# Kernel tuning notes

Measured on AMD Instinct MI355X. Metric: run time of the kernel, lower is better.

The kernel has to match this reference:

```python
import jax, jax.numpy as jnp
import numpy as np

DIMS = 1024
HEAD = 16
HEAD_DIM = DIMS // HEAD
MAX_ITERS = 3
THRESH = 0.01   # torch uses self.threshold.item() -> plain float, no grad
FACTOR = 0.1    # torch uses self.factor.item()
EPS = 1e-5


def _ln(x, w):
    # LayerNorm(bias=False): (x-mean)/sqrt(var+eps) * w
    m = jnp.mean(x, axis=-1, keepdims=True)
    xc = x - m
    v = jnp.mean(xc * xc, axis=-1, keepdims=True)
    return xc * jax.lax.rsqrt(v + EPS) * w


def _focus(xw, Wq, bq, Wk, Wv, bv, Wo, bo, lna_w, lnb_w,
           lq_w, lq_b, lk_w, lk_b, lv_w, lv_b):
    # xw: [B, S, DIMS]. NOTE: in the torch code xa is effectively ignored inside
    # create_qkv (k/v are computed from x due to the `xa is not None` branch bug),
    # so each window is pure self-attention on the query window.
    B, S, D = xw.shape
    xn = _ln(xw, lna_w)
    scale = HEAD_DIM ** -0.25
    q = (xn @ Wq.T + bq) * scale
    k = (xn @ Wk.T) * scale          # k Linear has no bias
    v = xn @ Wv.T + bv

    def shp(t):
        return t.reshape(B, S, HEAD, HEAD_DIM).transpose(0, 2, 1, 3)  # [B,h,S,d]

    q, k, v = shp(q), shp(k), shp(v)
    q = _ln(q, lnb_w)
    k = _ln(k, lnb_w)

    causal = jnp.tril(jnp.ones((S, S), dtype=bool))
    neg = jnp.finfo(jnp.float32).min
    inv_sqrt_d = 1.0 / np.sqrt(HEAD_DIM).astype(np.float32)

    q_cur = q
    prev = jnp.zeros_like(q)
    attn_out = jnp.zeros_like(q)
    done = jnp.array(False)

    # eff_span == S here (span_len >= win_size, ctx % win_size == 0), so the
    # [:eff_span] slices in torch are no-ops. Unrolled loop with where-gating
    # reproduces the data-dependent early exit and stays reverse-differentiable.
    for it in range(MAX_ITERS):
        qp = _ln(q_cur @ lq_w.T + lq_b, lnb_w)
        kp = _ln(k @ lk_w.T + lk_b, lnb_w)
        vp = v @ lv_w.T + lv_b
        s = jnp.einsum('bhqd,bhkd->bhqk', qp, kp) * inv_sqrt_d
        s = jnp.where(causal, s, neg)
        a = jax.nn.softmax(s, axis=-1)
        o = jnp.einsum('bhqk,bhkd->bhqd', a, vp)
        # torch: permute(0,2,1,3).flatten(2) -> [B,S,h*d], then (buggy) raw
        # view(B, HEAD, S, HEAD_DIM) with NO transpose; out_proj is NOT applied
        # in this branch. Reproduced faithfully.
        iter_out = (o.transpose(0, 2, 1, 3)
                     .reshape(B, S, HEAD * HEAD_DIM)
                     .reshape(B, HEAD, S, HEAD_DIM))
        diff = jnp.mean(jnp.abs(iter_out - prev))
        conv = jnp.logical_and(diff < THRESH + FACTOR * diff, it > 0)
        attn_out = jnp.where(done, attn_out, iter_out)
        upd = jnp.logical_or(done, conv)
        q_cur = jnp.where(upd, q_cur, q_cur + iter_out)
        prev = jnp.where(upd, prev, iter_out)
        done = upd

    out = attn_out.transpose(0, 2, 1, 3).reshape(B, S, D)
    return out @ Wo.T + bo


def setup_inputs() -> dict:
    key = jax.random.key(0)
    ks = jax.random.split(key, 10)

    def w(k, shape, s=0.02):
        return jax.random.normal(k, shape, dtype=jnp.float32) * s

    return {
        'x': jax.random.normal(ks[0], (4, 4096, DIMS), dtype=jnp.float32),
        'Wq': w(ks[1], (DIMS, DIMS)), 'bq': jnp.zeros((DIMS,), jnp.float32),
        'Wk': w(ks[2], (DIMS, DIMS)),
        'Wv': w(ks[3], (DIMS, DIMS)), 'bv': jnp.zeros((DIMS,), jnp.float32),
        'Wo': w(ks[4], (DIMS, DIMS)), 'bo': jnp.zeros((DIMS,), jnp.float32),
        'lna_w': jnp.ones((DIMS,), jnp.float32),
        'lnb_w': jnp.ones((HEAD_DIM,), jnp.float32),
        'lq_w': w(ks[5], (HEAD_DIM, HEAD_DIM), 0.1), 'lq_b': jnp.zeros((HEAD_DIM,), jnp.float32),
        'lk_w': w(ks[6], (HEAD_DIM, HEAD_DIM), 0.1), 'lk_b': jnp.zeros((HEAD_DIM,), jnp.float32),
        'lv_w': w(ks[7], (HEAD_DIM, HEAD_DIM), 0.1), 'lv_b': jnp.zeros((HEAD_DIM,), jnp.float32),
        'win_size': 512,
        'span_len': 1024,
    }


def reference(x, Wq, bq, Wk, Wv, bv, Wo, bo, lna_w, lnb_w,
              lq_w, lq_b, lk_w, lk_b, lv_w, lv_b, win_size, span_len):
    # span_len only influences eff_span in torch; with span_len >= win_size it
    # has no effect on the math (k/v come from the query window due to the bug).
    b, ctx, dims = x.shape
    nwin = ctx // win_size  # ctx chosen divisible by win_size
    xw = x.reshape(b, nwin, win_size, dims).transpose(1, 0, 2, 3)  # [nwin,B,W,D]
    f = lambda xx: _focus(xx, Wq, bq, Wk, Wv, bv, Wo, bo, lna_w, lnb_w,
                          lq_w, lq_b, lk_w, lk_b, lv_w, lv_b)
    out = jax.vmap(f)(xw)  # per-window convergence test, matching torch
    return out.transpose(1, 0, 2, 3).reshape(b, ctx, dims)
```

## Files before the change

kernel.cpp:

```cpp
#include <hip/hip_runtime.h>
#include <math.h>

#define DIMS   1024
#define NHEAD  16
#define HD     64
#define WIN    512
#define CTX    4096
#define NBATCH 4
#define NROWS  (NBATCH*CTX)
#define NUNITS (NROWS*NHEAD)
#define LNEPS  1e-5f
#define FIXSCALE 16777216.0

typedef __attribute__((ext_vector_type(8))) short bf16x8;
typedef __attribute__((ext_vector_type(4))) float f32x4;

__device__ __forceinline__ float4 ld4(const float* p) { return *reinterpret_cast<const float4*>(p); }
__device__ __forceinline__ void st4(float* p, float4 v) { *reinterpret_cast<float4*>(p) = v; }

__device__ __forceinline__ float wave_sum64(float v) {
#pragma unroll
    for (int off = 32; off; off >>= 1) v += __shfl_xor(v, off, 64);
    return v;
}
__device__ __forceinline__ float grp16_sum(float v) {
    v += __shfl_xor(v, 1, 64);
    v += __shfl_xor(v, 2, 64);
    v += __shfl_xor(v, 4, 64);
    v += __shfl_xor(v, 8, 64);
    return v;
}

__device__ __forceinline__ unsigned bf16_rn_bits(float x) {
    unsigned u = __float_as_uint(x);
    return (u + 0x7fffu + ((u >> 16) & 1u)) >> 16;
}
__device__ __forceinline__ unsigned pack_hl(float x) {
    unsigned h = bf16_rn_bits(x);
    float hf = __uint_as_float(h << 16);
    unsigned l = bf16_rn_bits(x - hf);
    return (h << 16) | (l & 0xffffu);
}

__device__ __forceinline__ unsigned cvtpk_bf16(float a, float b) {
    unsigned r;
    asm volatile("v_cvt_pk_bf16_f32 %0, %1, %2" : "=v"(r) : "v"(a), "v"(b));
    return r;
}
__device__ __forceinline__ void split_pair(float a, float b, unsigned& hw, unsigned& lw) {
    hw = cvtpk_bf16(a, b);
    float ha = __uint_as_float(hw << 16);
    float hb = __uint_as_float(hw & 0xffff0000u);
    lw = cvtpk_bf16(a - ha, b - hb);
}

__device__ __forceinline__ int swzo(int row, int kbyte) {
    return ((row << 7) + kbyte) ^ ((row & 7) << 4);
}

__global__ __launch_bounds__(256)
void ln1024_pack_kernel(const float* __restrict__ x, const float* __restrict__ w,
                        unsigned* __restrict__ outp) {
    int r = blockIdx.x;
    int tid = threadIdx.x;
    const float* xr = x + (size_t)r * DIMS;
    float4 v = ld4(xr + (tid << 2));
    __shared__ float red[8];
    float s = wave_sum64(v.x + v.y + v.z + v.w);
    int wv = tid >> 6, lane = tid & 63;
    if (lane == 0) red[wv] = s;
    __syncthreads();
    float mean = (red[0] + red[1] + red[2] + red[3]) * (1.0f / DIMS);
    float dx = v.x - mean, dy = v.y - mean, dz = v.z - mean, dw = v.w - mean;
    float ss = wave_sum64(dx*dx + dy*dy + dz*dz + dw*dw);
    if (lane == 0) red[4 + wv] = ss;
    __syncthreads();
    float inv = rsqrtf((red[4] + red[5] + red[6] + red[7]) * (1.0f / DIMS) + LNEPS);
    float4 wv4 = ld4(w + (tid << 2));
    uint4 pk;
    pk.x = pack_hl(dx * inv * wv4.x);
    pk.y = pack_hl(dy * inv * wv4.y);
    pk.z = pack_hl(dz * inv * wv4.z);
    pk.w = pack_hl(dw * inv * wv4.w);
    *reinterpret_cast<uint4*>(outp + (size_t)r * DIMS + (tid << 2)) = pk;
}

__global__ __launch_bounds__(256, 2)
void gemm_hl_kernel(const unsigned* __restrict__ Ahl, const float* __restrict__ W,
                    const float* __restrict__ bias, float* __restrict__ Cm,
                    float alpha, int has_bias) {
    __shared__ short Ah[128 * 64], Al[128 * 64], Wh[128 * 64], Wl[128 * 64];
    int tid = threadIdx.x;
    int wid = tid >> 6, lane = tid & 63;
    int wm = (wid >> 1) << 6, wn = (wid & 1) << 6;
    int g4 = lane >> 4, l16 = lane & 15;
    int m0 = blockIdx.x << 7, n0 = blockIdx.y << 7;

    f32x4 acc[4][4] = {};

    int orow[4], okb[4];
#pragma unroll
    for (int j = 0; j < 4; ++j) {
        int oc = tid + (j << 8);
        orow[j] = oc >> 3;
        okb[j] = (oc & 7) << 4;
    }

    for (int k0 = 0; k0 < 1024; k0 += 64) {
        uint4 a0[4], a1[4];
        float4 w0[4], w1[4];
#pragma unroll
        for (int j = 0; j < 4; ++j) {
            const unsigned* ap = Ahl + (size_t)(m0 + orow[j]) * 1024 + k0 + (okb[j] >> 1);
            a0[j] = *reinterpret_cast<const uint4*>(ap);
            a1[j] = *reinterpret_cast<const uint4*>(ap + 4);
            const float* wp = W + (size_t)(n0 + orow[j]) * 1024 + k0 + (okb[j] >> 1);
            w0[j] = *reinterpret_cast<const float4*>(wp);
            w1[j] = *reinterpret_cast<const float4*>(wp + 4);
        }
        __syncthreads();
#pragma unroll
        for (int j = 0; j < 4; ++j) {
            int off = swzo(orow[j], okb[j]);
            uint4 hi, lo;
            hi.x = __byte_perm(a0[j].x, a0[j].y, 0x7632);
            hi.y = __byte_perm(a0[j].z, a0[j].w, 0x7632);
            hi.z = __byte_perm(a1[j].x, a1[j].y, 0x7632);
            hi.w = __byte_perm(a1[j].z, a1[j].w, 0x7632);
            lo.x = __byte_perm(a0[j].x, a0[j].y, 0x5410);
            lo.y = __byte_perm(a0[j].z, a0[j].w, 0x5410);
            lo.z = __byte_perm(a1[j].x, a1[j].y, 0x5410);
            lo.w = __byte_perm(a1[j].z, a1[j].w, 0x5410);
            *reinterpret_cast<uint4*>(reinterpret_cast<char*>(Ah) + off) = hi;
            *reinterpret_cast<uint4*>(reinterpret_cast<char*>(Al) + off) = lo;

            float xs[8];
            *reinterpret_cast<float4*>(&xs[0]) = w0[j];
            *reinterpret_cast<float4*>(&xs[4]) = w1[j];
            uint4 hw4, lw4;
            unsigned* hwp = &hw4.x;
            unsigned* lwp = &lw4.x;
#pragma unroll
            for (int p = 0; p < 4; ++p) {
                unsigned u0 = __float_as_uint(xs[2*p]);
                unsigned u1 = __float_as_uint(xs[2*p + 1]);
                unsigned h0 = (u0 + 0x8000u) >> 16;
                unsigned h1 = (u1 + 0x8000u) >> 16;
                float l0 = xs[2*p]     - __uint_as_float(h0 << 16);
                float l1 = xs[2*p + 1] - __uint_as_float(h1 << 16);
                unsigned lb0 = (__float_as_uint(l0) + 0x8000u) >> 16;
                unsigned lb1 = (__float_as_uint(l1) + 0x8000u) >> 16;
                hwp[p] = h0 | (h1 << 16);
                lwp[p] = lb0 | (lb1 << 16);
            }
            *reinterpret_cast<uint4*>(reinterpret_cast<char*>(Wh) + off) = hw4;
            *reinterpret_cast<uint4*>(reinterpret_cast<char*>(Wl) + off) = lw4;
        }
        __syncthreads();

#pragma unroll
        for (int kk = 0; kk < 2; ++kk) {
            bf16x8 afh[4], afl[4], wfh[4], wfl[4];
#pragma unroll
            for (int mt = 0; mt < 4; ++mt) {
                int row = wm + (mt << 4) + l16;
                int off = ((row << 7) + (kk << 6) + (g4 << 4)) ^ ((row & 7) << 4);
                afh[mt] = *reinterpret_cast<const bf16x8*>(reinterpret_cast<const char*>(Ah) + off);
                afl[mt] = *reinterpret_cast<const bf16x8*>(reinterpret_cast<const char*>(Al) + off);
            }
#pragma unroll
            for (int nt = 0; nt < 4; ++nt) {
                int row = wn + (nt << 4) + l16;
                int off = ((row << 7) + (kk << 6) + (g4 << 4)) ^ ((row & 7) << 4);
                wfh[nt] = *reinterpret_cast<const bf16x8*>(reinterpret_cast<const char*>(Wh) + off);
                wfl[nt] = *reinterpret_cast<const bf16x8*>(reinterpret_cast<const char*>(Wl) + off);
            }
#pragma unroll
            for (int mt = 0; mt < 4; ++mt)
#pragma unroll
                for (int nt = 0; nt < 4; ++nt) {
                    acc[mt][nt] = __builtin_amdgcn_mfma_f32_16x16x32_bf16(afh[mt], wfh[nt], acc[mt][nt], 0, 0, 0);
                    acc[mt][nt] = __builtin_amdgcn_mfma_f32_16x16x32_bf16(afl[mt], wfh[nt], acc[mt][nt], 0, 0, 0);
                    acc[mt][nt] = __builtin_amdgcn_mfma_f32_16x16x32_bf16(afh[mt], wfl[nt], acc[mt][nt], 0, 0, 0);
                }
        }
    }

#pragma unroll
    for (int mt = 0; mt < 4; ++mt)
#pragma unroll
        for (int nt = 0; nt < 4; ++nt) {
            int col = n0 + wn + (nt << 4) + l16;
            float bb = has_bias ? bias[col] : 0.0f;
#pragma unroll
            for (int r = 0; r < 4; ++r) {
                int row = m0 + wm + (mt << 4) + (g4 << 2) + r;
                Cm[(size_t)row * DIMS + col] = alpha * (acc[mt][nt][r] + bb);
            }
        }
}

__global__ __launch_bounds__(256)
void headln_kernel(float* __restrict__ q, float* __restrict__ k,
                   const float* __restrict__ lnw) {
    int gw = (blockIdx.x << 2) + (threadIdx.x >> 6);
    int lane = threadIdx.x & 63;
    size_t idx = ((size_t)gw << 6) + lane;
    float wgt = lnw[lane];
    {
        float v = q[idx];
        float mean = wave_sum64(v) * (1.0f / 64.0f);
        float d = v - mean;
        float var = wave_sum64(d * d) * (1.0f / 64.0f);
        q[idx] = d * rsqrtf(var + LNEPS) * wgt;
    }
    {
        float v = k[idx];
        float mean = wave_sum64(v) * (1.0f / 64.0f);
        float d = v - mean;
        float var = wave_sum64(d * d) * (1.0f / 64.0f);
        k[idx] = d * rsqrtf(var + LNEPS) * wgt;
    }
}

__global__ __launch_bounds__(256)
void proj64_khl_kernel(const float* __restrict__ inp, const float* __restrict__ W,
                       const float* __restrict__ Wb, const float* __restrict__ lnw,
                       unsigned* __restrict__ plane) {
    int u0 = blockIdx.x << 6;
    __shared__ float As[64][68];
    __shared__ float Bs[64][68];
    int tid = threadIdx.x;
    for (int e = tid; e < 4096; e += 256) Bs[e & 63][e >> 6] = W[e];
    for (int e = tid; e < 1024; e += 256) {
        int row = e >> 4;
        int col = (e & 15) << 2;
        float4 v = ld4(inp + ((size_t)(u0 + row) << 6) + col);
        As[col + 0][row] = v.x; As[col + 1][row] = v.y;
        As[col + 2][row] = v.z; As[col + 3][row] = v.w;
    }
    __syncthreads();
    int tm = tid >> 4, tn = tid & 15;
    float acc[4][4] = {};
#pragma unroll
    for (int k = 0; k < 64; ++k) {
        float4 av = ld4(&As[k][tm << 2]);
        float4 bv = ld4(&Bs[k][tn << 2]);
        float aa[4] = {av.x, av.y, av.z, av.w};
        float bb[4] = {bv.x, bv.y, bv.z, bv.w};
#pragma unroll
        for (int mm = 0; mm < 4; ++mm)
#pragma unroll
            for (int nn = 0; nn < 4; ++nn)
                acc[mm][nn] = fmaf(aa[mm], bb[nn], acc[mm][nn]);
    }
    float bb4[4] = {Wb[(tn << 2) + 0], Wb[(tn << 2) + 1], Wb[(tn << 2) + 2], Wb[(tn << 2) + 3]};
    float lw4[4] = {lnw[(tn << 2) + 0], lnw[(tn << 2) + 1], lnw[(tn << 2) + 2], lnw[(tn << 2) + 3]};
#pragma unroll
    for (int mm = 0; mm < 4; ++mm) {
        float o0 = acc[mm][0] + bb4[0], o1 = acc[mm][1] + bb4[1];
        float o2 = acc[mm][2] + bb4[2], o3 = acc[mm][3] + bb4[3];
        float mean = grp16_sum(o0 + o1 + o2 + o3) * (1.0f / 64.0f);
        float d0 = o0 - mean, d1 = o1 - mean, d2 = o2 - mean, d3 = o3 - mean;
        float var = grp16_sum(d0*d0 + d1*d1 + d2*d2 + d3*d3) * (1.0f / 64.0f);
        float inv = rsqrtf(var + LNEPS);
        o0 = d0 * inv * lw4[0]; o1 = d1 * inv * lw4[1];
        o2 = d2 * inv * lw4[2]; o3 = d3 * inv * lw4[3];
        int u_p = u0 + (tm << 2) + mm;
        int r = u_p >> 4, h = u_p & 15;
        int s = r & 511;
        int ua = ((r >> 9) << 4) + h;
        size_t punit = (size_t)ua * 512 + s;
        uint4 pk;
        pk.x = pack_hl(o0); pk.y = pack_hl(o1); pk.z = pack_hl(o2); pk.w = pack_hl(o3);
        *reinterpret_cast<uint4*>(plane + (punit << 6) + (tn << 2)) = pk;
    }
}

__global__ __launch_bounds__(256)
void proj64_vthl_kernel(const float* __restrict__ inp, const float* __restrict__ W,
                        const float* __restrict__ Wb, unsigned* __restrict__ plane) {
    int u0 = blockIdx.x << 6;
    __shared__ float As[64][68];
    __shared__ float Bs[64][68];
    int tid = threadIdx.x;
    for (int e = tid; e < 4096; e += 256) Bs[e & 63][e >> 6] = W[e];
    for (int e = tid; e < 1024; e += 256) {
        int row = e >> 4;
        int col = (e & 15) << 2;
        float4 v = ld4(inp + ((size_t)(u0 + row) << 6) + col);
        As[col + 0][row] = v.x; As[col + 1][row] = v.y;
        As[col + 2][row] = v.z; As[col + 3][row] = v.w;
    }
    __syncthreads();
    int tm = tid >> 4, tn = tid & 15;
    float acc[4][4] = {};
#pragma unroll
    for (int k = 0; k < 64; ++k) {
        float4 av = ld4(&As[k][tm << 2]);
        float4 bv = ld4(&Bs[k][tn << 2]);
        float aa[4] = {av.x, av.y, av.z, av.w};
        float bb[4] = {bv.x, bv.y, bv.z, bv.w};
#pragma unroll
        for (int mm = 0; mm < 4; ++mm)
#pragma unroll
            for (int nn = 0; nn < 4; ++nn)
                acc[mm][nn] = fmaf(aa[mm], bb[nn], acc[mm][nn]);
    }
    float bb4[4] = {Wb[(tn << 2) + 0], Wb[(tn << 2) + 1], Wb[(tn << 2) + 2], Wb[(tn << 2) + 3]};
#pragma unroll
    for (int mm = 0; mm < 4; ++mm) {
        int u_p = u0 + (tm << 2) + mm;
        int r = u_p >> 4, h = u_p & 15;
        int s = r & 511;
        int ua = ((r >> 9) << 4) + h;
        size_t base = ((size_t)(ua * 8 + (s >> 6)) << 12) + (s & 63);
#pragma unroll
        for (int nn = 0; nn < 4; ++nn) {
            int d = (tn << 2) + nn;
            plane[base + ((size_t)d << 6)] = pack_hl(acc[mm][nn] + bb4[nn]);
        }
    }
}

template<int DIFF, int USE_CONV>
__global__ __launch_bounds__(256)
void attn_mfma_kernel(const float* __restrict__ qacc, const unsigned* __restrict__ khl,
                      const unsigned* __restrict__ vthl, float* __restrict__ o_io,
                      const float* __restrict__ lqw, const float* __restrict__ lqb,
                      const float* __restrict__ lnw,
                      unsigned long long* __restrict__ diff_acc,
                      const int* __restrict__ conv) {
    __shared__ short kh[64][72], kl[64][72], vh[64][72], vl[64][72];
    __shared__ float dred[4];

    int blk = blockIdx.x;
    int u = blk & 511;
    int t = 7 - (blk >> 9);
    int h = u & 15;
    int w = (u >> 4) & 7;
    int b = u >> 7;
    if (USE_CONV && conv[w]) return;
    int rowbase = b * CTX + w * WIN;
    int col0 = h * HD;
    int tid = threadIdx.x;
    int wv = tid >> 6;
    int lane = tid & 63;
    int g4 = lane >> 4;
    int qcol = lane & 15;
    int q_loc = (wv << 4) + qcol;
    int selhi = g4 >> 1;

    const unsigned* kbase = khl + (((size_t)u * 512) << 6);
    const unsigned* vbase = vthl + (((size_t)u * 8) << 12);

    uint4 kpre[4], vpre[4];
#pragma unroll
    for (int rr = 0; rr < 4; ++rr) {
        int row = (wv << 4) + (rr << 2) + g4;
        kpre[rr] = *reinterpret_cast<const uint4*>(kbase + ((size_t)row << 6) + (qcol << 2));
        vpre[rr] = *reinterpret_cast<const uint4*>(vbase + ((size_t)row << 6) + (qcol << 2));
    }

#pragma unroll
    for (int rr = 0; rr < 4; ++rr) {
        int row = (wv << 4) + (rr << 2) + g4;
        float4 v = ld4(lqw + (row << 6) + (qcol << 2));
        unsigned h0, l0, h1, l1;
        split_pair(v.x, v.y, h0, l0);
        split_pair(v.z, v.w, h1, l1);
        *reinterpret_cast<uint2*>(&kh[row][qcol << 2]) = make_uint2(h0, h1);
        *reinterpret_cast<uint2*>(&kl[row][qcol << 2]) = make_uint2(l0, l1);
    }

    bf16x8 bqh[2], bql[2];
    {
        const float* qrow = qacc + (size_t)(rowbase + (t << 6) + q_loc) * DIMS + col0;
#pragma unroll
        for (int kb = 0; kb < 2; ++kb) {
            float4 x0 = ld4(qrow + (kb << 5) + (g4 << 3));
            float4 x1 = ld4(qrow + (kb << 5) + (g4 << 3) + 4);
            unsigned hws[4], lws[4];
            split_pair(x0.x, x0.y, hws[0], lws[0]);
            split_pair(x0.z, x0.w, hws[1], lws[1]);
            split_pair(x1.x, x1.y, hws[2], lws[2]);
            split_pair(x1.z, x1.w, hws[3], lws[3]);
#pragma unroll
            for (int p2 = 0; p2 < 4; ++p2) {
                reinterpret_cast<unsigned*>(&bqh[kb])[p2] = hws[p2];
                reinterpret_cast<unsigned*>(&bql[kb])[p2] = lws[p2];
            }
        }
    }
    __syncthreads();

    f32x4 qpa[4] = {{0,0,0,0},{0,0,0,0},{0,0,0,0},{0,0,0,0}};
    __builtin_amdgcn_s_setprio(1);
#pragma unroll
    for (int jt = 0; jt < 4; ++jt) {
        int arow = (jt << 4) + qcol;
#pragma unroll
        for (int kb = 0; kb < 2; ++kb) {
            bf16x8 ah = *reinterpret_cast<const bf16x8*>(&kh[arow][(kb << 5) + (g4 << 3)]);
            bf16x8 al = *reinterpret_cast<const bf16x8*>(&kl[arow][(kb << 5) + (g4 << 3)]);
            qpa[jt] = __builtin_amdgcn_mfma_f32_16x16x32_bf16(ah, bqh[kb], qpa[jt], 0, 0, 0);
            qpa[jt] = __builtin_amdgcn_mfma_f32_16x16x32_bf16(al, bqh[kb], qpa[jt], 0, 0, 0);
            qpa[jt] = __builtin_amdgcn_mfma_f32_16x16x32_bf16(ah, bql[kb], qpa[jt], 0, 0, 0);
        }
    }
    __builtin_amdgcn_s_setprio(0);

    float vals[16];
    float s1 = 0.0f;
#pragma unroll
    for (int jt = 0; jt < 4; ++jt) {
        float4 b4 = ld4(lqb + (jt << 4) + (g4 << 2));
        const float* b4p = reinterpret_cast<const float*>(&b4);
#pragma unroll
        for (int r = 0; r < 4; ++r) {
            float v = qpa[jt][r] + b4p[r];
            vals[(jt << 2) + r] = v;
            s1 += v;
        }
    }
    s1 += __shfl_xor(s1, 16, 64);
    s1 += __shfl_xor(s1, 32, 64);
    float mean = s1 * (1.0f / 64.0f);
    float s2 = 0.0f;
#pragma unroll
    for (int e = 0; e < 16; ++e) { float d = vals[e] - mean; vals[e] = d; s2 += d * d; }
    s2 += __shfl_xor(s2, 16, 64);
    s2 += __shfl_xor(s2, 32, 64);
    float inv = rsqrtf(s2 * (1.0f / 64.0f) + LNEPS);
#pragma unroll
    for (int jt = 0; jt < 4; ++jt) {
        float4 w4 = ld4(lnw + (jt << 4) + (g4 << 2));
        const float* w4p = reinterpret_cast<const float*>(&w4);
#pragma unroll
        for (int r = 0; r < 4; ++r) vals[(jt << 2) + r] *= inv * w4p[r];
    }

    bf16x8 qfh[2], qfl[2];
    {
        unsigned hw[8], lw[8];
#pragma unroll
        for (int jt = 0; jt < 4; ++jt) {
            split_pair(vals[(jt << 2) + 0], vals[(jt << 2) + 1], hw[(jt << 1) + 0], lw[(jt << 1) + 0]);
            split_pair(vals[(jt << 2) + 2], vals[(jt << 2) + 3], hw[(jt << 1) + 1], lw[(jt << 1) + 1]);
        }
#pragma unroll
        for (int kb = 0; kb < 2; ++kb)
#pragma unroll
            for (int ip = 0; ip < 4; ++ip) {
                int srcl = (((g4 & 1) << 1) + (ip >> 1)) * 16 + qcol;
                unsigned hA = __shfl(hw[(kb << 2) + (ip & 1)], srcl, 64);
                unsigned hB = __shfl(hw[(kb << 2) + 2 + (ip & 1)], srcl, 64);
                unsigned lA = __shfl(lw[(kb << 2) + (ip & 1)], srcl, 64);
                unsigned lB = __shfl(lw[(kb << 2) + 2 + (ip & 1)], srcl, 64);
                reinterpret_cast<unsigned*>(&qfh[kb])[ip] = selhi ? hB : hA;
                reinterpret_cast<unsigned*>(&qfl[kb])[ip] = selhi ? lB : lA;
            }
    }
    __syncthreads();

    float m_r = -INFINITY, l_r = 0.0f;
    f32x4 oacc[4] = {{0,0,0,0},{0,0,0,0},{0,0,0,0},{0,0,0,0}};

    for (int c = 0; c <= t; ++c) {
#pragma unroll
        for (int rr = 0; rr < 4; ++rr) {
            int row = (wv << 4) + (rr << 2) + g4;
            uint4 pk = kpre[rr];
            unsigned* khp = reinterpret_cast<unsigned*>(&kh[row][qcol << 2]);
            khp[0] = __byte_perm(pk.x, pk.y, 0x7632);
            khp[1] = __byte_perm(pk.z, pk.w, 0x7632);
            unsigned* klp = reinterpret_cast<unsigned*>(&kl[row][qcol << 2]);
            klp[0] = __byte_perm(pk.x, pk.y, 0x5410);
            klp[1] = __byte_perm(pk.z, pk.w, 0x5410);
            uint4 pv = vpre[rr];
            unsigned* vhp = reinterpret_cast<unsigned*>(&vh[row][qcol << 2]);
            vhp[0] = __byte_perm(pv.x, pv.y, 0x7632);
            vhp[1] = __byte_perm(pv.z, pv.w, 0x7632);
            unsigned* vlp = reinterpret_cast<unsigned*>(&vl[row][qcol << 2]);
            vlp[0] = __byte_perm(pv.x, pv.y, 0x5410);
            vlp[1] = __byte_perm(pv.z, pv.w, 0x5410);
        }
        if (c < t) {
            const unsigned* ksrc = kbase + (((size_t)(c + 1) * 64) << 6);
            const unsigned* vsrc = vbase + (((size_t)(c + 1)) << 12);
#pragma unroll
            for (int rr = 0; rr < 4; ++rr) {
                int row = (wv << 4) + (rr << 2) + g4;
                kpre[rr] = *reinterpret_cast<const uint4*>(ksrc + ((size_t)row << 6) + (qcol << 2));
                vpre[rr] = *reinterpret_cast<const uint4*>(vsrc + ((size_t)row << 6) + (qcol << 2));
            }
        }
        __syncthreads();

        f32x4 sacc[4] = {{0,0,0,0},{0,0,0,0},{0,0,0,0},{0,0,0,0}};
        __builtin_amdgcn_s_setprio(1);
#pragma unroll
        for (int jt = 0; jt < 4; ++jt) {
            int jrow = (jt << 4) + qcol;
#pragma unroll
            for (int kb = 0; kb < 2; ++kb) {
                bf16x8 ah = *reinterpret_cast<const bf16x8*>(&kh[jrow][(kb << 5) + (g4 << 3)]);
                bf16x8 al = *reinterpret_cast<const bf16x8*>(&kl[jrow][(kb << 5) + (g4 << 3)]);
                sacc[jt] = __builtin_amdgcn_mfma_f32_16x16x32_bf16(ah, qfh[kb], sacc[jt], 0, 0, 0);
                sacc[jt] = __builtin_amdgcn_mfma_f32_16x16x32_bf16(al, qfh[kb], sacc[jt], 0, 0, 0);
                sacc[jt] = __builtin_amdgcn_mfma_f32_16x16x32_bf16(ah, qfl[kb], sacc[jt], 0, 0, 0);
            }
        }
        __builtin_amdgcn_s_setprio(0);

        float sv[16];
        float mx = -3.0e38f;
#pragma unroll
        for (int jt = 0; jt < 4; ++jt)
#pragma unroll
            for (int r = 0; r < 4; ++r) {
                float s = sacc[jt][r] * 0.125f;
                if (c == t) {
                    int j_loc = (jt << 4) + (g4 << 2) + r;
                    if (j_loc > q_loc) s = -3.0e38f;
                }
                sv[(jt << 2) + r] = s;
                mx = fmaxf(mx, s);
            }
        mx = fmaxf(mx, __shfl_xor(mx, 16, 64));
        mx = fmaxf(mx, __shfl_xor(mx, 32, 64));
        float mnew = fmaxf(m_r, mx);
        float ps = 0.0f;
#pragma unroll
        for (int e = 0; e < 16; ++e) {
            float p = __expf(sv[e] - mnew);
            sv[e] = p;
            ps += p;
        }
        ps += __shfl_xor(ps, 16, 64);
        ps += __shfl_xor(ps, 32, 64);
        float ef = __expf(m_r - mnew);
        l_r = l_r * ef + ps;
        m_r = mnew;
#pragma unroll
        for (int dt = 0; dt < 4; ++dt) oacc[dt] *= ef;

        unsigned hwp[8], lwp[8];
#pragma unroll
        for (int jt = 0; jt < 4; ++jt) {
            split_pair(sv[(jt << 2) + 0], sv[(jt << 2) + 1], hwp[(jt << 1) + 0], lwp[(jt << 1) + 0]);
            split_pair(sv[(jt << 2) + 2], sv[(jt << 2) + 3], hwp[(jt << 1) + 1], lwp[(jt << 1) + 1]);
        }

        __builtin_amdgcn_s_setprio(1);
#pragma unroll
        for (int kb2 = 0; kb2 < 2; ++kb2) {
            bf16x8 ph, pl;
#pragma unroll
            for (int ip = 0; ip < 4; ++ip) {
                int srcl = (((g4 & 1) << 1) + (ip >> 1)) * 16 + qcol;
                unsigned hA = __shfl(hwp[(kb2 << 2) + (ip & 1)], srcl, 64);
                unsigned hB = __shfl(hwp[(kb2 << 2) + 2 + (ip & 1)], srcl, 64);
                unsigned lA = __shfl(lwp[(kb2 << 2) + (ip & 1)], srcl, 64);
                unsigned lB = __shfl(lwp[(kb2 << 2) + 2 + (ip & 1)], srcl, 64);
                reinterpret_cast<unsigned*>(&ph)[ip] = selhi ? hB : hA;
                reinterpret_cast<unsigned*>(&pl)[ip] = selhi ? lB : lA;
            }
#pragma unroll
            for (int dt = 0; dt < 4; ++dt) {
                int drow = (dt << 4) + qcol;
                bf16x8 ah = *reinterpret_cast<const bf16x8*>(&vh[drow][(kb2 << 5) + (g4 << 3)]);
                bf16x8 al = *reinterpret_cast<const bf16x8*>(&vl[drow][(kb2 << 5) + (g4 << 3)]);
                oacc[dt] = __builtin_amdgcn_mfma_f32_16x16x32_bf16(ah, ph, oacc[dt], 0, 0, 0);
                oacc[dt] = __builtin_amdgcn_mfma_f32_16x16x32_bf16(al, ph, oacc[dt], 0, 0, 0);
                oacc[dt] = __builtin_amdgcn_mfma_f32_16x16x32_bf16(ah, pl, oacc[dt], 0, 0, 0);
            }
        }
        __builtin_amdgcn_s_setprio(0);
        __syncthreads();
    }

    float invl = 1.0f / l_r;
    float dsum = 0.0f;
    float* orow = o_io + (size_t)(rowbase + (t << 6) + q_loc) * DIMS + col0;
#pragma unroll
    for (int dt = 0; dt < 4; ++dt) {
        float4 ov = make_float4(oacc[dt][0] * invl, oacc[dt][1] * invl,
                                oacc[dt][2] * invl, oacc[dt][3] * invl);
        float* addr = orow + (dt << 4) + (g4 << 2);
        if (DIFF) {
            float4 pv4 = ld4(addr);
            dsum += fabsf(ov.x - pv4.x) + fabsf(ov.y - pv4.y)
                  + fabsf(ov.z - pv4.z) + fabsf(ov.w - pv4.w);
        }
        st4(addr, ov);
    }
    if (DIFF) {
        float s = wave_sum64(dsum);
        if (lane == 0) dred[wv] = s;
        __syncthreads();
        if (tid == 0) {
            double tot = (double)(dred[0] + dred[1] + dred[2] + dred[3]);
            unsigned long long q = (unsigned long long)(tot * FIXSCALE + 0.5);
            atomicAdd(&diff_acc[w], q);
        }
    }
}

__global__ __launch_bounds__(256)
void scatter_add_kernel(float* __restrict__ qacc, const float* __restrict__ o) {
    size_t gid = (size_t)blockIdx.x * 256 + threadIdx.x;
    size_t flat = gid << 2;
    int uu = (int)(flat >> 6);
    int col = (int)(flat & 63);
    int r = uu >> 4, h = uu & 15;
    int s = r & 511;
    int rb = r - s;
    size_t src = ((size_t)(rb + h * 32 + (s >> 4)) << 10)
               + (size_t)((s & 15) << 6) + col;
    float4 a = ld4(qacc + flat);
    float4 bv = ld4(o + src);
    st4(qacc + flat, make_float4(a.x + bv.x, a.y + bv.y, a.z + bv.z, a.w + bv.w));
}

__global__ void init_ctrl_kernel(unsigned long long* __restrict__ dacc,
                                 int* __restrict__ conv) {
    int i = threadIdx.x;
    if (i < 8) { dacc[i] = 0ULL; conv[i] = 0; }
}

__global__ void conv_from_acc_kernel(const unsigned long long* __restrict__ dacc,
                                     int* __restrict__ conv) {
    int w = threadIdx.x;
    if (w < 8) {
        float mean = (float)((double)dacc[w] * (1.0 / (FIXSCALE * 2097152.0)));
        conv[w] = (mean < 0.01f + 0.1f * mean) ? 1 : 0;
    }
}

__global__ __launch_bounds__(256)
void unscramble_pack_kernel(const float* __restrict__ src, unsigned* __restrict__ outp) {
    size_t gid = (size_t)blockIdx.x * 256 + threadIdx.x;
    size_t flat = gid << 2;
    int r = (int)(flat >> 10);
    int e = (int)(flat & 1023);
    int h2 = e >> 6, d2 = e & 63;
    int s2 = r & 511;
    int rb = r - s2;
    size_t sidx = ((size_t)(rb + h2 * 32 + (s2 >> 4)) << 10) + (size_t)((s2 & 15) << 6) + d2;
    float4 v = ld4(src + sidx);
    uint4 pk;
    pk.x = pack_hl(v.x); pk.y = pack_hl(v.y); pk.z = pack_hl(v.z); pk.w = pack_hl(v.w);
    *reinterpret_cast<uint4*>(outp + flat) = pk;
}

extern "C" void kernel_launch(void* const* d_in, const int* in_sizes, int n_in,
                              void* d_out, int out_size, void* d_ws, size_t ws_size,
                              hipStream_t stream) {
    (void)in_sizes; (void)n_in; (void)out_size; (void)ws_size;
    const float* x   = (const float*)d_in[0];
    const float* Wq  = (const float*)d_in[1];
    const float* bq  = (const float*)d_in[2];
    const float* Wk  = (const float*)d_in[3];
    const float* Wv  = (const float*)d_in[4];
    const float* bv  = (const float*)d_in[5];
    const float* Wo  = (const float*)d_in[6];
    const float* bo  = (const float*)d_in[7];
    const float* lna = (const float*)d_in[8];
    const float* lnb = (const float*)d_in[9];
    const float* lqw = (const float*)d_in[10];
    const float* lqb = (const float*)d_in[11];
    const float* lkw = (const float*)d_in[12];
    const float* lkb = (const float*)d_in[13];
    const float* lvw = (const float*)d_in[14];
    const float* lvb = (const float*)d_in[15];

    const size_t BUF = (size_t)NROWS * DIMS;
    unsigned long long* dacc = (unsigned long long*)d_ws;
    int* conv = (int*)(dacc + 8);
    float* R1 = (float*)((char*)d_ws + 4096);
    float* R2 = R1 + BUF;
    float* R3 = R2 + BUF;
    float* E  = (float*)d_out;

    const float scale = 0.35355339059327373f;

    ln1024_pack_kernel<<<NROWS, 256, 0, stream>>>(x, lna, (unsigned*)R2);

    dim3 gg(NROWS / 128, DIMS / 128);
    gemm_hl_kernel<<<gg, 256, 0, stream>>>((const unsigned*)R2, Wq, bq, R1, scale, 1);
    gemm_hl_kernel<<<gg, 256, 0, stream>>>((const unsigned*)R2, Wk, bq, E,  scale, 0);
    gemm_hl_kernel<<<gg, 256, 0, stream>>>((const unsigned*)R2, Wv, bv, R3, 1.0f, 1);

    headln_kernel<<<NUNITS / 4, 256, 0, stream>>>(R1, E, lnb);

    proj64_khl_kernel<<<NUNITS / 64, 256, 0, stream>>>(E, lkw, lkb, lnb, (unsigned*)R2);
    proj64_vthl_kernel<<<NUNITS / 64, 256, 0, stream>>>(R3, lvw, lvb, (unsigned*)E);

    init_ctrl_kernel<<<1, 64, 0, stream>>>(dacc, conv);

    const unsigned* KHL = (const unsigned*)R2;
    const unsigned* VTHL = (const unsigned*)E;

    attn_mfma_kernel<0, 0><<<512 * 8, 256, 0, stream>>>(R1, KHL, VTHL, R3, lqw, lqb, lnb, dacc, conv);
    scatter_add_kernel<<<NROWS * DIMS / 4 / 256, 256, 0, stream>>>(R1, R3);
    attn_mfma_kernel<1, 0><<<512 * 8, 256, 0, stream>>>(R1, KHL, VTHL, R3, lqw, lqb, lnb, dacc, conv);
    conv_from_acc_kernel<<<1, 64, 0, stream>>>(dacc, conv);
    scatter_add_kernel<<<NROWS * DIMS / 4 / 256, 256, 0, stream>>>(R1, R3);
    attn_mfma_kernel<0, 1><<<512 * 8, 256, 0, stream>>>(R1, KHL, VTHL, R3, lqw, lqb, lnb, dacc, conv);

    unscramble_pack_kernel<<<NROWS * DIMS / 4 / 256, 256, 0, stream>>>(R3, (unsigned*)R2);
    gemm_hl_kernel<<<gg, 256, 0, stream>>>((const unsigned*)R2, Wo, bo, (float*)d_out, 1.0f, 1);
}
```

Measured before the change: 1.134 ms.

## Fuse head LayerNorm into QK GEMM epilogue and restructure attention K/V staging

```diff
diff --git a/kernel.cpp b/kernel.cpp
--- a/kernel.cpp
+++ b/kernel.cpp
@@ -85,10 +85,11 @@
     *reinterpret_cast<uint4*>(outp + (size_t)r * DIMS + (tid << 2)) = pk;
 }
 
+template<int DO_HLN>
 __global__ __launch_bounds__(256, 2)
 void gemm_hl_kernel(const unsigned* __restrict__ Ahl, const float* __restrict__ W,
                     const float* __restrict__ bias, float* __restrict__ Cm,
-                    float alpha, int has_bias) {
+                    float alpha, int has_bias, const float* __restrict__ lnw) {
     __shared__ short Ah[128 * 64], Al[128 * 64], Wh[128 * 64], Wl[128 * 64];
     int tid = threadIdx.x;
     int wid = tid >> 6, lane = tid & 63;
@@ -186,40 +187,50 @@
         }
     }
 
-#pragma unroll
-    for (int mt = 0; mt < 4; ++mt)
-#pragma unroll
-        for (int nt = 0; nt < 4; ++nt) {
-            int col = n0 + wn + (nt << 4) + l16;
-            float bb = has_bias ? bias[col] : 0.0f;
+    if (DO_HLN) {
+        float bb[4];
+#pragma unroll
+        for (int nt = 0; nt < 4; ++nt)
+            bb[nt] = has_bias ? bias[n0 + wn + (nt << 4) + l16] : 0.0f;
+        float lw4[4];
+#pragma unroll
+        for (int nt = 0; nt < 4; ++nt) lw4[nt] = lnw[(nt << 4) + l16];
+#pragma unroll
+        for (int mt = 0; mt < 4; ++mt)
 #pragma unroll
             for (int r = 0; r < 4; ++r) {
+                float v[4];
+                float s1 = 0.0f;
+#pragma unroll
+                for (int nt = 0; nt < 4; ++nt) {
+                    v[nt] = alpha * (acc[mt][nt][r] + bb[nt]);
+                    s1 += v[nt];
+                }
+                s1 = grp16_sum(s1);
+                float mean = s1 * (1.0f / 64.0f);
+                float s2 = 0.0f;
+#pragma unroll
+                for (int nt = 0; nt < 4; ++nt) { v[nt] -= mean; s2 += v[nt] * v[nt]; }
+                s2 = grp16_sum(s2);
+                float inv = rsqrtf(s2 * (1.0f / 64.0f) + LNEPS);
                 int row = m0 + wm + (mt << 4) + (g4 << 2) + r;
-                Cm[(size_t)row * DIMS + col] = alpha * (acc[mt][nt][r] + bb);
-            }
-        }
-}
-
-__global__ __launch_bounds__(256)
-void headln_kernel(float* __restrict__ q, float* __restrict__ k,
-                   const float* __restrict__ lnw) {
-    int gw = (blockIdx.x << 2) + (threadIdx.x >> 6);
-    int lane = threadIdx.x & 63;
-    size_t idx = ((size_t)gw << 6) + lane;
-    float wgt = lnw[lane];
-    {
-        float v = q[idx];
-        float mean = wave_sum64(v) * (1.0f / 64.0f);
-        float d = v - mean;
-        float var = wave_sum64(d * d) * (1.0f / 64.0f);
-        q[idx] = d * rsqrtf(var + LNEPS) * wgt;
-    }
-    {
-        float v = k[idx];
-        float mean = wave_sum64(v) * (1.0f / 64.0f);
-        float d = v - mean;
-        float var = wave_sum64(d * d) * (1.0f / 64.0f);
-        k[idx] = d * rsqrtf(var + LNEPS) * wgt;
+#pragma unroll
+                for (int nt = 0; nt < 4; ++nt)
+                    Cm[(size_t)row * DIMS + n0 + wn + (nt << 4) + l16] = v[nt] * inv * lw4[nt];
+            }
+    } else {
+#pragma unroll
+        for (int mt = 0; mt < 4; ++mt)
+#pragma unroll
+            for (int nt = 0; nt < 4; ++nt) {
+                int col = n0 + wn + (nt << 4) + l16;
+                float bb = has_bias ? bias[col] : 0.0f;
+#pragma unroll
+                for (int r = 0; r < 4; ++r) {
+                    int row = m0 + wm + (mt << 4) + (g4 << 2) + r;
+                    Cm[(size_t)row * DIMS + col] = alpha * (acc[mt][nt][r] + bb);
+                }
+            }
     }
 }
 
@@ -331,7 +342,7 @@
                       const float* __restrict__ lnw,
                       unsigned long long* __restrict__ diff_acc,
                       const int* __restrict__ conv) {
-    __shared__ short kh[64][72], kl[64][72], vh[64][72], vl[64][72];
+    __shared__ short kh[2][64][72], kl[2][64][72];
     __shared__ float dred[4];
 
     int blk = blockIdx.x;
@@ -352,14 +363,13 @@
     int selhi = g4 >> 1;
 
     const unsigned* kbase = khl + (((size_t)u * 512) << 6);
-    const unsigned* vbase = vthl + (((size_t)u * 8) << 12);
-
-    uint4 kpre[4], vpre[4];
+    const unsigned* vptr = vthl + (((size_t)u * 8) << 12) + (qcol << 6) + (g4 << 3);
+
+    uint4 kpre[4];
 #pragma unroll
     for (int rr = 0; rr < 4; ++rr) {
         int row = (wv << 4) + (rr << 2) + g4;
         kpre[rr] = *reinterpret_cast<const uint4*>(kbase + ((size_t)row << 6) + (qcol << 2));
-        vpre[rr] = *reinterpret_cast<const uint4*>(vbase + ((size_t)row << 6) + (qcol << 2));
     }
 
 #pragma unroll
@@ -369,8 +379,8 @@
         unsigned h0, l0, h1, l1;
         split_pair(v.x, v.y, h0, l0);
         split_pair(v.z, v.w, h1, l1);
-        *reinterpret_cast<uint2*>(&kh[row][qcol << 2]) = make_uint2(h0, h1);
-        *reinterpret_cast<uint2*>(&kl[row][qcol << 2]) = make_uint2(l0, l1);
+        *reinterpret_cast<uint2*>(&kh[0][row][qcol << 2]) = make_uint2(h0, h1);
+        *reinterpret_cast<uint2*>(&kl[0][row][qcol << 2]) = make_uint2(l0, l1);
     }
 
     bf16x8 bqh[2], bql[2];
@@ -401,8 +411,8 @@
         int arow = (jt << 4) + qcol;
 #pragma unroll
         for (int kb = 0; kb < 2; ++kb) {
-            bf16x8 ah = *reinterpret_cast<const bf16x8*>(&kh[arow][(kb << 5) + (g4 << 3)]);
-            bf16x8 al = *reinterpret_cast<const bf16x8*>(&kl[arow][(kb << 5) + (g4 << 3)]);
+            bf16x8 ah = *reinterpret_cast<const bf16x8*>(&kh[0][arow][(kb << 5) + (g4 << 3)]);
+            bf16x8 al = *reinterpret_cast<const bf16x8*>(&kl[0][arow][(kb << 5) + (g4 << 3)]);
             qpa[jt] = __builtin_amdgcn_mfma_f32_16x16x32_bf16(ah, bqh[kb], qpa[jt], 0, 0, 0);
             qpa[jt] = __builtin_amdgcn_mfma_f32_16x16x32_bf16(al, bqh[kb], qpa[jt], 0, 0, 0);
             qpa[jt] = __builtin_amdgcn_mfma_f32_16x16x32_bf16(ah, bql[kb], qpa[jt], 0, 0, 0);
@@ -463,55 +473,61 @@
     }
     __syncthreads();
 
+#pragma unroll
+    for (int rr = 0; rr < 4; ++rr) {
+        int row = (wv << 4) + (rr << 2) + g4;
+        uint4 pk = kpre[rr];
+        unsigned* khp = reinterpret_cast<unsigned*>(&kh[0][row][qcol << 2]);
+        khp[0] = __byte_perm(pk.x, pk.y, 0x7632);
+        khp[1] = __byte_perm(pk.z, pk.w, 0x7632);
+        unsigned* klp = reinterpret_cast<unsigned*>(&kl[0][row][qcol << 2]);
+        klp[0] = __byte_perm(pk.x, pk.y, 0x5410);
+        klp[1] = __byte_perm(pk.z, pk.w, 0x5410);
+    }
+    __syncthreads();
+
     float m_r = -INFINITY, l_r = 0.0f;
     f32x4 oacc[4] = {{0,0,0,0},{0,0,0,0},{0,0,0,0},{0,0,0,0}};
 
     for (int c = 0; c <= t; ++c) {
-#pragma unroll
-        for (int rr = 0; rr < 4; ++rr) {
-            int row = (wv << 4) + (rr << 2) + g4;
-            uint4 pk = kpre[rr];
-            unsigned* khp = reinterpret_cast<unsigned*>(&kh[row][qcol << 2]);
-            khp[0] = __byte_perm(pk.x, pk.y, 0x7632);
-            khp[1] = __byte_perm(pk.z, pk.w, 0x7632);
-            unsigned* klp = reinterpret_cast<unsigned*>(&kl[row][qcol << 2]);
-            klp[0] = __byte_perm(pk.x, pk.y, 0x5410);
-            klp[1] = __byte_perm(pk.z, pk.w, 0x5410);
-            uint4 pv = vpre[rr];
-            unsigned* vhp = reinterpret_cast<unsigned*>(&vh[row][qcol << 2]);
-            vhp[0] = __byte_perm(pv.x, pv.y, 0x7632);
-            vhp[1] = __byte_perm(pv.z, pv.w, 0x7632);
-            unsigned* vlp = reinterpret_cast<unsigned*>(&vl[row][qcol << 2]);
-            vlp[0] = __byte_perm(pv.x, pv.y, 0x5410);
-            vlp[1] = __byte_perm(pv.z, pv.w, 0x5410);
-        }
+        int X = c & 1;
+        uint4 va[8];
+#pragma unroll
+        for (int dt = 0; dt < 4; ++dt) {
+            va[(dt << 1) + 0] = *reinterpret_cast<const uint4*>(vptr + (dt << 10));
+            va[(dt << 1) + 1] = *reinterpret_cast<const uint4*>(vptr + (dt << 10) + 4);
+        }
+
+        f32x4 sacc[4] = {{0,0,0,0},{0,0,0,0},{0,0,0,0},{0,0,0,0}};
+        __builtin_amdgcn_s_setprio(1);
+#pragma unroll
+        for (int jt = 0; jt < 4; ++jt) {
+            int jrow = (jt << 4) + qcol;
+#pragma unroll
+            for (int kb = 0; kb < 2; ++kb) {
+                bf16x8 ah = *reinterpret_cast<const bf16x8*>(&kh[X][jrow][(kb << 5) + (g4 << 3)]);
+                bf16x8 al = *reinterpret_cast<const bf16x8*>(&kl[X][jrow][(kb << 5) + (g4 << 3)]);
+                sacc[jt] = __builtin_amdgcn_mfma_f32_16x16x32_bf16(ah, qfh[kb], sacc[jt], 0, 0, 0);
+                sacc[jt] = __builtin_amdgcn_mfma_f32_16x16x32_bf16(al, qfh[kb], sacc[jt], 0, 0, 0);
+                sacc[jt] = __builtin_amdgcn_mfma_f32_16x16x32_bf16(ah, qfl[kb], sacc[jt], 0, 0, 0);
+            }
+        }
+        __builtin_amdgcn_s_setprio(0);
+
         if (c < t) {
             const unsigned* ksrc = kbase + (((size_t)(c + 1) * 64) << 6);
-            const unsigned* vsrc = vbase + (((size_t)(c + 1)) << 12);
 #pragma unroll
             for (int rr = 0; rr < 4; ++rr) {
                 int row = (wv << 4) + (rr << 2) + g4;
                 kpre[rr] = *reinterpret_cast<const uint4*>(ksrc + ((size_t)row << 6) + (qcol << 2));
-                vpre[rr] = *reinterpret_cast<const uint4*>(vsrc + ((size_t)row << 6) + (qcol << 2));
-            }
-        }
-        __syncthreads();
-
-        f32x4 sacc[4] = {{0,0,0,0},{0,0,0,0},{0,0,0,0},{0,0,0,0}};
-        __builtin_amdgcn_s_setprio(1);
-#pragma unroll
-        for (int jt = 0; jt < 4; ++jt) {
-            int jrow = (jt << 4) + qcol;
-#pragma unroll
-            for (int kb = 0; kb < 2; ++kb) {
-                bf16x8 ah = *reinterpret_cast<const bf16x8*>(&kh[jrow][(kb << 5) + (g4 << 3)]);
-                bf16x8 al = *reinterpret_cast<const bf16x8*>(&kl[jrow][(kb << 5) + (g4 << 3)]);
-                sacc[jt] = __builtin_amdgcn_mfma_f32_16x16x32_bf16(ah, qfh[kb], sacc[jt], 0, 0, 0);
-                sacc[jt] = __builtin_amdgcn_mfma_f32_16x16x32_bf16(al, qfh[kb], sacc[jt], 0, 0, 0);
-                sacc[jt] = __builtin_amdgcn_mfma_f32_16x16x32_bf16(ah, qfl[kb], sacc[jt], 0, 0, 0);
-            }
-        }
-        __builtin_amdgcn_s_setprio(0);
+            }
+        }
+        uint4 vb[8];
+#pragma unroll
+        for (int dt = 0; dt < 4; ++dt) {
+            vb[(dt << 1) + 0] = *reinterpret_cast<const uint4*>(vptr + (dt << 10) + 32);
+            vb[(dt << 1) + 1] = *reinterpret_cast<const uint4*>(vptr + (dt << 10) + 36);
+        }
 
         float sv[16];
         float mx = -3.0e38f;
@@ -529,21 +545,24 @@
             }
         mx = fmaxf(mx, __shfl_xor(mx, 16, 64));
         mx = fmaxf(mx, __shfl_xor(mx, 32, 64));
-        float mnew = fmaxf(m_r, mx);
+        if (!__all(mx <= m_r + 8.0f)) {
+            float mnew = fmaxf(m_r, mx);
+            float ef = __expf(m_r - mnew);
+            l_r *= ef;
+#pragma unroll
+            for (int dt = 0; dt < 4; ++dt) oacc[dt] *= ef;
+            m_r = mnew;
+        }
         float ps = 0.0f;
 #pragma unroll
         for (int e = 0; e < 16; ++e) {
-            float p = __expf(sv[e] - mnew);
+            float p = __expf(sv[e] - m_r);
             sv[e] = p;
             ps += p;
         }
         ps += __shfl_xor(ps, 16, 64);
         ps += __shfl_xor(ps, 32, 64);
-        float ef = __expf(m_r - mnew);
-        l_r = l_r * ef + ps;
-        m_r = mnew;
-#pragma unroll
-        for (int dt = 0; dt < 4; ++dt) oacc[dt] *= ef;
+        l_r += ps;
 
         unsigned hwp[8], lwp[8];
 #pragma unroll
@@ -566,17 +585,41 @@
                 reinterpret_cast<unsigned*>(&ph)[ip] = selhi ? hB : hA;
                 reinterpret_cast<unsigned*>(&pl)[ip] = selhi ? lB : lA;
             }
+            const uint4* vv = (kb2 == 0) ? va : vb;
 #pragma unroll
             for (int dt = 0; dt < 4; ++dt) {
-                int drow = (dt << 4) + qcol;
-                bf16x8 ah = *reinterpret_cast<const bf16x8*>(&vh[drow][(kb2 << 5) + (g4 << 3)]);
-                bf16x8 al = *reinterpret_cast<const bf16x8*>(&vl[drow][(kb2 << 5) + (g4 << 3)]);
+                uint4 p0 = vv[(dt << 1) + 0];
+                uint4 p1 = vv[(dt << 1) + 1];
+                bf16x8 ah, al;
+                reinterpret_cast<unsigned*>(&ah)[0] = __byte_perm(p0.x, p0.y, 0x7632);
+                reinterpret_cast<unsigned*>(&ah)[1] = __byte_perm(p0.z, p0.w, 0x7632);
+                reinterpret_cast<unsigned*>(&ah)[2] = __byte_perm(p1.x, p1.y, 0x7632);
+                reinterpret_cast<unsigned*>(&ah)[3] = __byte_perm(p1.z, p1.w, 0x7632);
+                reinterpret_cast<unsigned*>(&al)[0] = __byte_perm(p0.x, p0.y, 0x5410);
+                reinterpret_cast<unsigned*>(&al)[1] = __byte_perm(p0.z, p0.w, 0x5410);
+                reinterpret_cast<unsigned*>(&al)[2] = __byte_perm(p1.x, p1.y, 0x5410);
+                reinterpret_cast<unsigned*>(&al)[3] = __byte_perm(p1.z, p1.w, 0x5410);
                 oacc[dt] = __builtin_amdgcn_mfma_f32_16x16x32_bf16(ah, ph, oacc[dt], 0, 0, 0);
                 oacc[dt] = __builtin_amdgcn_mfma_f32_16x16x32_bf16(al, ph, oacc[dt], 0, 0, 0);
                 oacc[dt] = __builtin_amdgcn_mfma_f32_16x16x32_bf16(ah, pl, oacc[dt], 0, 0, 0);
             }
         }
         __builtin_amdgcn_s_setprio(0);
+
+        if (c < t) {
+#pragma unroll
+            for (int rr = 0; rr < 4; ++rr) {
+                int row = (wv << 4) + (rr << 2) + g4;
+                uint4 pk = kpre[rr];
+                unsigned* khp = reinterpret_cast<unsigned*>(&kh[X ^ 1][row][qcol << 2]);
+                khp[0] = __byte_perm(pk.x, pk.y, 0x7632);
+                khp[1] = __byte_perm(pk.z, pk.w, 0x7632);
+                unsigned* klp = reinterpret_cast<unsigned*>(&kl[X ^ 1][row][qcol << 2]);
+                klp[0] = __byte_perm(pk.x, pk.y, 0x5410);
+                klp[1] = __byte_perm(pk.z, pk.w, 0x5410);
+            }
+        }
+        vptr += 4096;
         __syncthreads();
     }
 
@@ -688,11 +731,9 @@
     ln1024_pack_kernel<<<NROWS, 256, 0, stream>>>(x, lna, (unsigned*)R2);
 
     dim3 gg(NROWS / 128, DIMS / 128);
-    gemm_hl_kernel<<<gg, 256, 0, stream>>>((const unsigned*)R2, Wq, bq, R1, scale, 1);
-    gemm_hl_kernel<<<gg, 256, 0, stream>>>((const unsigned*)R2, Wk, bq, E,  scale, 0);
-    gemm_hl_kernel<<<gg, 256, 0, stream>>>((const unsigned*)R2, Wv, bv, R3, 1.0f, 1);
-
-    headln_kernel<<<NUNITS / 4, 256, 0, stream>>>(R1, E, lnb);
+    gemm_hl_kernel<1><<<gg, 256, 0, stream>>>((const unsigned*)R2, Wq, bq, R1, scale, 1, lnb);
+    gemm_hl_kernel<1><<<gg, 256, 0, stream>>>((const unsigned*)R2, Wk, bq, E,  scale, 0, lnb);
+    gemm_hl_kernel<0><<<gg, 256, 0, stream>>>((const unsigned*)R2, Wv, bv, R3, 1.0f, 1, lnb);
 
     proj64_khl_kernel<<<NUNITS / 64, 256, 0, stream>>>(E, lkw, lkb, lnb, (unsigned*)R2);
     proj64_vthl_kernel<<<NUNITS / 64, 256, 0, stream>>>(R3, lvw, lvb, (unsigned*)E);
@@ -710,5 +751,5 @@
     attn_mfma_kernel<0, 1><<<512 * 8, 256, 0, stream>>>(R1, KHL, VTHL, R3, lqw, lqb, lnb, dacc, conv);
 
     unscramble_pack_kernel<<<NROWS * DIMS / 4 / 256, 256, 0, stream>>>(R3, (unsigned*)R2);
-    gemm_hl_kernel<<<gg, 256, 0, stream>>>((const unsigned*)R2, Wo, bo, (float*)d_out, 1.0f, 1);
-}
+    gemm_hl_kernel<0><<<gg, 256, 0, stream>>>((const unsigned*)R2, Wo, bo, (float*)d_out, 1.0f, 1, lnb);
+}
```

Result: no change. 1.148 ms (median of 2 runs) (+1.2%).
